# Kernel optimization log

Hardware: AMD Instinct MI355X
Metric: run time of the kernel (lower is better)

Reference implementation:

```python
import jax, jax.numpy as jnp
import numpy as np

B, T, SC, D, N, K, H = 2, 1024, 1024, 2048, 16, 4, 128
SOFTCAP = 50.0
BIG_NEG = -2.3819763e38


def _apply_rope(x, positions, max_wavelength=10_000):
    # x: [B, T, heads, H], positions: [B, T]
    h = x.shape[-1]
    freq_exponents = (2.0 / h) * jnp.arange(h // 2, dtype=jnp.float32)
    timescale = max_wavelength ** freq_exponents
    radians = positions[..., None].astype(jnp.float32) / timescale  # [B,T,H/2]
    radians = radians[..., None, :]  # [B,T,1,H/2]
    sin, cos = jnp.sin(radians), jnp.cos(radians)
    x1, x2 = jnp.split(x, 2, axis=-1)
    out = jnp.concatenate([x1 * cos - x2 * sin, x2 * cos + x1 * sin], axis=-1)
    return out.astype(x.dtype)


def setup_inputs() -> dict:
    key = jax.random.key(0)
    ks = jax.random.split(key, 6)
    x = jax.random.normal(ks[0], (B, T, D), jnp.float32)
    # new-token positions follow the cache: SC .. SC+T-1
    positions = jnp.broadcast_to(SC + jnp.arange(T, dtype=jnp.int32), (B, T))
    # causal mask over concatenated [cache | new] keys
    q_pos = SC + jnp.arange(T)
    k_pos = jnp.arange(SC + T)
    attn_mask = jnp.broadcast_to(
        (k_pos[None, :] <= q_pos[:, None])[None, None], (B, 1, T, SC + T)
    )
    cache_k = jax.random.normal(ks[1], (B, SC, K, H), jnp.float32)
    cache_v = jax.random.normal(ks[2], (B, SC, K, H), jnp.float32)
    wq = jax.random.normal(ks[3], (N, D, H), jnp.float32) * (D ** -0.5)
    wkv = jax.random.normal(ks[4], (2, K, D, H), jnp.float32) * (D ** -0.5)
    wout = jax.random.normal(ks[5], (N, H, D), jnp.float32) * ((N * H) ** -0.5)
    return {"x": x, "positions": positions, "attn_mask": attn_mask,
            "cache_k": cache_k, "cache_v": cache_v,
            "wq": wq, "wkv": wkv, "wout": wout}


def reference(x, positions, attn_mask, cache_k, cache_v, wq, wkv, wout):
    dtype = x.dtype
    h = wq.shape[-1]
    k_heads = wkv.shape[1]
    # projections (GQA path: separate q and fused kv einsums)
    q = jnp.einsum('BTD,NDH->BTNH', x, wq.astype(dtype))
    kv = jnp.einsum('BSD,cKDH->cBSKH', x, wkv.astype(dtype))
    k, v = kv[0], kv[1]
    # RoPE then query pre-attn scaling (rsqrt_head_dim)
    q = _apply_rope(q, positions) * (h ** -0.5)
    k = _apply_rope(k, positions)
    # KV cache concat along sequence axis
    k = jnp.concatenate([cache_k.astype(dtype), k], axis=1)
    v = jnp.concatenate([cache_v.astype(dtype), v], axis=1)
    b, t, n, _ = q.shape
    g = n // k_heads
    q = q.reshape(b, t, k_heads, g, h)  # B T K G H
    logits = jnp.einsum('BTKGH,BSKH->BKGTS', q, k,
                        preferred_element_type=jnp.float32)
    # tanh logits softcap
    logits = jnp.tanh(logits / SOFTCAP) * SOFTCAP
    masked = jnp.where(attn_mask[:, :, None, :, :], logits, BIG_NEG)
    probs = jax.nn.softmax(masked, axis=-1).astype(dtype)
    encoded = jnp.einsum('BKGTS,BSKH->BTKGH', probs, v)
    encoded = encoded.reshape(b, t, n, h)
    out = jnp.einsum('BTNH,NHD->BTD', encoded, wout.astype(dtype))
    return out
```

## Files before the change

### kernel.cpp

```cpp
#include <hip/hip_runtime.h>
#include <stdint.h>
#include <stddef.h>


typedef __bf16 bf16_t;
typedef __bf16 bf16x8 __attribute__((ext_vector_type(8)));
typedef __bf16 bf16x4 __attribute__((ext_vector_type(4)));
typedef float  f32x4  __attribute__((ext_vector_type(4)));

#define GLDS16(gsrc, ldst)                                                      \
  __builtin_amdgcn_global_load_lds(                                             \
      (const __attribute__((address_space(1))) void*)(gsrc),                    \
      (__attribute__((address_space(3))) void*)(ldst), 16, 0, 0)

__global__ __launch_bounds__(256)
void k_prep(const float* __restrict__ x, bf16_t* __restrict__ xb,
            const float* __restrict__ wq, const float* __restrict__ wkv,
            const float* __restrict__ wout,
            bf16_t* __restrict__ w1t, bf16_t* __restrict__ wot) {
  __shared__ bf16_t tile[64][65];
  const int blk = blockIdx.x;
  const int tid = threadIdx.x;
  if (blk < 4096) {
    int i = blk * 256 + tid;
    f32x4 v = *(const f32x4*)(x + (size_t)i * 4);
    bf16x4 o;
    o[0] = (bf16_t)v[0]; o[1] = (bf16_t)v[1]; o[2] = (bf16_t)v[2]; o[3] = (bf16_t)v[3];
    *(bf16x4*)(xb + (size_t)i * 4) = o;
    return;
  }
  const float* s; bf16_t* d; int R, C, bx, by;
  if (blk < 5120) {
    int local = blk - 4096;
    int z = local >> 6, rem = local & 63;
    by = rem >> 1; bx = rem & 1;
    R = 2048; C = 128;
    s = wq + (size_t)z * 2048 * 128;
    d = w1t + (size_t)z * 128 * 2048;
  } else if (blk < 5632) {
    int local = blk - 5120;
    int z = local >> 6, rem = local & 63;
    by = rem >> 1; bx = rem & 1;
    R = 2048; C = 128;
    s = wkv + (size_t)z * 2048 * 128;
    d = w1t + (size_t)2048 * 2048 + (size_t)z * 128 * 2048;
  } else {
    int local = blk - 5632;
    bx = local & 31; by = local >> 5;
    R = 2048; C = 2048;
    s = wout; d = wot;
  }
  const int c0 = bx * 64, r0 = by * 64;
#pragma unroll
  for (int it = 0; it < 16; ++it) {
    int idx = it * 256 + tid;
    int rl = idx >> 6, cl = idx & 63;
    tile[rl][cl] = (bf16_t)s[(size_t)(r0 + rl) * C + (c0 + cl)];
  }
  __syncthreads();
#pragma unroll
  for (int it = 0; it < 16; ++it) {
    int idx = it * 256 + tid;
    int cl = idx >> 6, rl = idx & 63;
    d[(size_t)(c0 + cl) * R + (r0 + rl)] = tile[rl][cl];
  }
}

template <typename CT>
__global__ __launch_bounds__(512)
void k_gemm_bt(const bf16_t* __restrict__ A, const bf16_t* __restrict__ Bt,
               CT* __restrict__ C, int M, int N, int Kd) {
  __shared__ char gsm[65536];
  const int tid = threadIdx.x;
  const int w = tid >> 6, l = tid & 63;
  const int wq = w & 3, wr = wq >> 1, wc = wq & 1, wk = w >> 2;
  const int lr = l & 15, lk = l >> 4;
  const int nwg = gridDim.x * gridDim.y;
  const int bid = blockIdx.y * gridDim.x + blockIdx.x;
  const int cpx = nwg >> 3;
  const int sid = (bid & 7) * cpx + (bid >> 3);
  const int row0 = (sid % gridDim.x) * 128;
  const int col0 = (sid / gridDim.x) * 128;

  auto stage = [&](int buf, int k0) {
#pragma unroll
    for (int inst = 0; inst < 2; ++inst) {
      uint32_t oo = (uint32_t)(inst * 8192 + tid * 16);
      uint32_t r  = oo >> 7;
      uint32_t kb = (oo ^ (((oo >> 7) & 7u) << 4)) & 127u;
      GLDS16((const char*)(A + (size_t)(row0 + r) * Kd + k0) + kb,
             gsm + buf * 16384 + oo);
      GLDS16((const char*)(Bt + (size_t)(col0 + r) * Kd + k0) + kb,
             gsm + 32768 + buf * 16384 + oo);
    }
  };

  f32x4 acc[4][4] = {};
  stage(0, 0);
  asm volatile("s_waitcnt vmcnt(0)" ::: "memory");
  __builtin_amdgcn_s_barrier();
  int cur = 0;
  for (int k0 = 0; k0 < Kd; k0 += 64) {
    if (k0 + 64 < Kd) stage(cur ^ 1, k0 + 64);
    const char* Ab = gsm + cur * 16384;
    const char* Bb = gsm + 32768 + cur * 16384;
    bf16x8 af[4], bfr[4];
#pragma unroll
    for (int m = 0; m < 4; ++m) {
      uint32_t r = (uint32_t)(wr * 64 + m * 16 + lr);
      uint32_t a = (r * 128u + (uint32_t)(wk * 64 + lk * 16)) ^ ((r & 7u) << 4);
      af[m] = *(const bf16x8*)(Ab + a);
    }
#pragma unroll
    for (int n = 0; n < 4; ++n) {
      uint32_t r = (uint32_t)(wc * 64 + n * 16 + lr);
      uint32_t a = (r * 128u + (uint32_t)(wk * 64 + lk * 16)) ^ ((r & 7u) << 4);
      bfr[n] = *(const bf16x8*)(Bb + a);
    }
    __builtin_amdgcn_s_setprio(1);
#pragma unroll
    for (int m = 0; m < 4; ++m)
#pragma unroll
      for (int n = 0; n < 4; ++n)
        acc[m][n] = __builtin_amdgcn_mfma_f32_16x16x32_bf16(af[m], bfr[n], acc[m][n], 0, 0, 0);
    __builtin_amdgcn_s_setprio(0);
    asm volatile("s_waitcnt vmcnt(0)" ::: "memory");
    __builtin_amdgcn_s_barrier();
    __builtin_amdgcn_sched_barrier(0);
    cur ^= 1;
  }
  if (wk == 1) {
#pragma unroll
    for (int m = 0; m < 4; ++m)
#pragma unroll
      for (int n = 0; n < 4; ++n)
        *(f32x4*)(gsm + wq * 16384 + ((m * 4 + n) * 64 + l) * 16) = acc[m][n];
  }
  __syncthreads();
  if (wk == 0) {
#pragma unroll
    for (int m = 0; m < 4; ++m) {
      const int rr = row0 + wr * 64 + m * 16 + lk * 4;
#pragma unroll
      for (int n = 0; n < 4; ++n) {
        f32x4 o = *(const f32x4*)(gsm + wq * 16384 + ((m * 4 + n) * 64 + l) * 16);
        const int cc = col0 + wc * 64 + n * 16 + lr;
        CT* cp = C + (size_t)rr * N + cc;
#pragma unroll
        for (int j = 0; j < 4; ++j) cp[(size_t)j * N] = (CT)(acc[m][n][j] + o[j]);
      }
    }
  }
}

__global__ __launch_bounds__(256)
void k_pre2(const bf16_t* __restrict__ qkv, const int* __restrict__ positions,
            const float* __restrict__ ck, const float* __restrict__ cv,
            bf16_t* __restrict__ Qr, bf16_t* __restrict__ Kf, bf16_t* __restrict__ Vt) {
  __shared__ char shm[16512];
  const int blk = blockIdx.x;
  const int tid = threadIdx.x;
  if (blk < 2048) {
    const int row = blk;
    const int b = row >> 10, t = row & 1023;
    float* cs = (float*)shm;
    float* sn = (float*)shm + 64;
    if (tid < 64) {
      float fe = (float)tid * (2.0f / 128.0f);
      float rad = (float)positions[row] * __builtin_amdgcn_exp2f(-fe * 13.287712379549449f);
      sn[tid] = __sinf(rad);
      cs[tid] = __cosf(rad);
    }
    __syncthreads();
    const bf16_t* rowp = qkv + (size_t)row * 3072;
    const float qs = 0.08838834764831845f;
#pragma unroll
    for (int it = 0; it < 8; ++it) {
      int idx = it * 256 + tid;
      int n = idx >> 7, hh = idx & 127;
      int hp = hh & 63;
      float x1 = (float)rowp[n * 128 + hp];
      float x2 = (float)rowp[n * 128 + 64 + hp];
      float o = (hh < 64) ? (x1 * cs[hp] - x2 * sn[hp]) : (x2 * cs[hp] + x1 * sn[hp]);
      Qr[(((size_t)b * 16 + n) * 1024 + t) * 128 + hh] = (bf16_t)(o * qs);
    }
#pragma unroll
    for (int it = 0; it < 2; ++it) {
      int idx = it * 256 + tid;
      int kh = idx >> 7, hh = idx & 127;
      int hp = hh & 63;
      float x1 = (float)rowp[2048 + kh * 128 + hp];
      float x2 = (float)rowp[2048 + kh * 128 + 64 + hp];
      float o = (hh < 64) ? (x1 * cs[hp] - x2 * sn[hp]) : (x2 * cs[hp] + x1 * sn[hp]);
      Kf[(((size_t)b * 4 + kh) * 2048 + 1024 + t) * 128 + hh] = (bf16_t)o;
    }
    return;
  }
  if (blk < 4096) {
    const int row = blk - 2048;
    const int b = row >> 10, s = row & 1023;
    const float* src = ck + (size_t)row * 512;
#pragma unroll
    for (int it = 0; it < 2; ++it) {
      int idx = it * 256 + tid;
      int kh = idx >> 7, hh = idx & 127;
      Kf[(((size_t)b * 4 + kh) * 2048 + s) * 128 + hh] = (bf16_t)src[idx];
    }
    return;
  }
  {
    const int local = blk - 4096;
    const int s0 = (local & 31) * 64;
    const int bk = local >> 5;
    const int b = bk >> 2, kh = bk & 3;
    bf16_t (*vt)[129] = (bf16_t(*)[129])shm;
#pragma unroll
    for (int it = 0; it < 32; ++it) {
      int idx = it * 256 + tid;
      int sl = idx >> 7, hh = idx & 127;
      int s = s0 + sl;
      vt[sl][hh] = (s < 1024)
        ? (bf16_t)cv[(((size_t)b * 1024 + s) * 4 + kh) * 128 + hh]
        : qkv[((size_t)b * 1024 + (s - 1024)) * 3072 + 2560 + kh * 128 + hh];
    }
    __syncthreads();
#pragma unroll
    for (int it = 0; it < 32; ++it) {
      int idx = it * 256 + tid;
      int hh = idx >> 6, sl = idx & 63;
      Vt[((size_t)bk * 128 + hh) * 2048 + s0 + sl] = vt[sl][hh];
    }
  }
}

__global__ __launch_bounds__(512)
void k_attn(const bf16_t* __restrict__ Qr, const bf16_t* __restrict__ Kf,
            const bf16_t* __restrict__ Vt, bf16_t* __restrict__ enc) {
  __shared__ char smem[74240];
  const int bid = blockIdx.y * gridDim.x + blockIdx.x;
  const int sid = (bid & 7) * 64 + (bid >> 3);
  const int qsel = sid & 15;
  const int bn = sid >> 4;
  const int qblk = ((bn >> 1) & 1) ? (15 - qsel) : qsel;
  const int b = bn >> 4, n = bn & 15;
  const int kh = n >> 2;
  const int tid = threadIdx.x;
  const int w = tid >> 6, l = tid & 63;
  const int qg = w & 1, sw = w >> 1;
  const int window = sw >> 1, hg = sw & 1;
  const int lr = l & 15, lk = l >> 4;
  const bf16_t* Kbase = Kf + ((size_t)b * 4 + kh) * 2048 * 128;
  const bf16_t* Vbase = Vt + ((size_t)b * 4 + kh) * 128 * 2048;
  float* psL = (float*)(smem + 73728);

  bf16x8 aq[2][4];
#pragma unroll
  for (int qf = 0; qf < 2; ++qf) {
    const bf16_t* qp = Qr + ((size_t)bn * 1024 + qblk * 64 + qg * 32 + qf * 16 + lr) * 128;
#pragma unroll
    for (int kk = 0; kk < 4; ++kk) aq[qf][kk] = *(const bf16x8*)(qp + kk * 32 + lk * 8);
  }

  auto stageK = [&](int buf, int s0) {
#pragma unroll
    for (int inst = 0; inst < 2; ++inst) {
      uint32_t oo = (uint32_t)(inst * 8192 + tid * 16);
      uint32_t r  = oo >> 8;
      uint32_t kb = (oo ^ (((oo >> 8) & 7u) << 4)) & 255u;
      GLDS16((const char*)(Kbase + (size_t)(s0 + r) * 128) + kb,
             smem + buf * 16384 + oo);
    }
  };
  auto stageV = [&](int buf, int s0) {
#pragma unroll
    for (int inst = 0; inst < 2; ++inst) {
      uint32_t oo = (uint32_t)(inst * 8192 + tid * 16);
      uint32_t r  = oo >> 7;
      uint32_t sb = (oo ^ (((oo >> 7) & 7u) << 4)) & 127u;
      GLDS16((const char*)(Vbase + (size_t)r * 2048 + s0) + sb,
             smem + 32768 + buf * 16384 + oo);
    }
  };

  char* Pq = smem + 65536 + qg * 4096;
  f32x4 acc[2][4] = {};
  float psum[2] = {0.f, 0.f};
  const int ntiles = 17 + qblk;
  const int qglob0 = 1024 + qblk * 64 + qg * 32 + lr;

  if (tid < 64) psL[tid] = 0.f;
  stageK(0, 0);
  stageV(0, 0);
  asm volatile("s_waitcnt vmcnt(0)" ::: "memory");
  __builtin_amdgcn_s_barrier();
  int cur = 0;

  for (int st = 0; st < ntiles; ++st) {
    const int s0 = st * 64;
    if (st + 1 < ntiles) {
      stageK(cur ^ 1, s0 + 64);
      stageV(cur ^ 1, s0 + 64);
    }
    const char* Kc = smem + cur * 16384;
    const char* Vc = smem + 32768 + cur * 16384;

    f32x4 sacc[2] = {};
    __builtin_amdgcn_s_setprio(1);
#pragma unroll
    for (int kk = 0; kk < 4; ++kk) {
      uint32_t r = (uint32_t)(sw * 16 + lr);
      uint32_t a = (r * 256u + (uint32_t)(kk * 64 + lk * 16)) ^ ((r & 7u) << 4);
      bf16x8 ak = *(const bf16x8*)(Kc + a);
      sacc[0] = __builtin_amdgcn_mfma_f32_16x16x32_bf16(ak, aq[0][kk], sacc[0], 0, 0, 0);
      sacc[1] = __builtin_amdgcn_mfma_f32_16x16x32_bf16(ak, aq[1][kk], sacc[1], 0, 0, 0);
    }
    __builtin_amdgcn_s_setprio(0);

    const bool last = (st == ntiles - 1);
#pragma unroll
    for (int qf = 0; qf < 2; ++qf) {
      const int q = qf * 16 + lr;
      bf16x4 pq;
#pragma unroll
      for (int j = 0; j < 4; ++j) {
        float lg = sacc[qf][j];
        float t  = lg * 1.4426950408889634f;
        float u  = 1.0f - (lg * lg) * (1.0f / 7500.0f);
        float p  = __builtin_amdgcn_exp2f(t * u);
        if (last) {
          int sg = s0 + sw * 16 + lk * 4 + j;
          if (sg > qglob0 + qf * 16) p = 0.0f;
        }
        psum[qf] += p;
        pq[j] = (bf16_t)p;
      }
      uint32_t a = ((uint32_t)(q * 128) + (uint32_t)(sw * 32 + lk * 8)) ^ (((uint32_t)lr & 7u) << 4);
      *(bf16x4*)(Pq + a) = pq;
    }
    asm volatile("s_waitcnt lgkmcnt(0)" ::: "memory");
    __builtin_amdgcn_s_barrier();
    __builtin_amdgcn_sched_barrier(0);

    {
      bf16x8 pa[2];
#pragma unroll
      for (int qf = 0; qf < 2; ++qf) {
        uint32_t a = ((uint32_t)((qf * 16 + lr) * 128) + (uint32_t)(window * 64 + lk * 16)) ^ (((uint32_t)lr & 7u) << 4);
        pa[qf] = *(const bf16x8*)(Pq + a);
      }
      __builtin_amdgcn_s_setprio(1);
#pragma unroll
      for (int i = 0; i < 4; ++i) {
        uint32_t h = (uint32_t)((hg * 4 + i) * 16 + lr);
        uint32_t va = (h * 128u + (uint32_t)(window * 64 + lk * 16)) ^ ((h & 7u) << 4);
        bf16x8 bv = *(const bf16x8*)(Vc + va);
        acc[0][i] = __builtin_amdgcn_mfma_f32_16x16x32_bf16(pa[0], bv, acc[0][i], 0, 0, 0);
        acc[1][i] = __builtin_amdgcn_mfma_f32_16x16x32_bf16(pa[1], bv, acc[1][i], 0, 0, 0);
      }
      __builtin_amdgcn_s_setprio(0);
    }
    asm volatile("s_waitcnt vmcnt(0)" ::: "memory");
    __builtin_amdgcn_s_barrier();
    __builtin_amdgcn_sched_barrier(0);
    cur ^= 1;
  }

  float ps0 = psum[0];
  ps0 += __shfl_xor(ps0, 16); ps0 += __shfl_xor(ps0, 32);
  float ps1 = psum[1];
  ps1 += __shfl_xor(ps1, 16); ps1 += __shfl_xor(ps1, 32);
  if (l < 16) {
    atomicAdd(&psL[qg * 32 + lr], ps0);
    atomicAdd(&psL[qg * 32 + 16 + lr], ps1);
  }
  float* accL = (float*)smem;
  if (window == 1) {
    char* sb = (char*)(accL) + (qg * 2 + hg) * 8192;
#pragma unroll
    for (int qf = 0; qf < 2; ++qf)
#pragma unroll
      for (int i = 0; i < 4; ++i) {
        uint32_t a = (uint32_t)(l * 128) + ((uint32_t)((qf * 4 + i) * 16) ^ (((uint32_t)l & 7u) << 4));
        *(f32x4*)(sb + a) = acc[qf][i];
      }
  }
  __syncthreads();
  if (window == 0) {
    char* sb = (char*)(accL) + (qg * 2 + hg) * 8192;
    float inv[2][4];
#pragma unroll
    for (int qf = 0; qf < 2; ++qf)
#pragma unroll
      for (int j = 0; j < 4; ++j)
        inv[qf][j] = 1.0f / (psL[qg * 32 + qf * 16 + lk * 4 + j] + 1e-30f);
#pragma unroll
    for (int qf = 0; qf < 2; ++qf) {
#pragma unroll
      for (int i = 0; i < 4; ++i) {
        uint32_t a = (uint32_t)(l * 128) + ((uint32_t)((qf * 4 + i) * 16) ^ (((uint32_t)l & 7u) << 4));
        f32x4 o2 = *(const f32x4*)(sb + a);
        const int col = n * 128 + (hg * 4 + i) * 16 + lr;
#pragma unroll
        for (int j = 0; j < 4; ++j) {
          int trow = qblk * 64 + qg * 32 + qf * 16 + lk * 4 + j;
          enc[((size_t)b * 1024 + trow) * 2048 + col] =
              (bf16_t)((acc[qf][i][j] + o2[j]) * inv[qf][j]);
        }
      }
    }
  }
}

extern "C" void kernel_launch(void* const* d_in, const int* in_sizes, int n_in,
                              void* d_out, int out_size, void* d_ws, size_t ws_size,
                              hipStream_t stream) {
  (void)in_sizes; (void)n_in; (void)out_size; (void)ws_size;
  const float* x    = (const float*)d_in[0];
  const int*   pos  = (const int*)d_in[1];
  const float* ck   = (const float*)d_in[3];
  const float* cv   = (const float*)d_in[4];
  const float* wq   = (const float*)d_in[5];
  const float* wkv  = (const float*)d_in[6];
  const float* wout = (const float*)d_in[7];
  float* out = (float*)d_out;

  char* p = (char*)d_ws;
  bf16_t* xb  = (bf16_t*)p; p += (size_t)2048 * 2048 * 2;
  bf16_t* w1t = (bf16_t*)p; p += (size_t)3072 * 2048 * 2;
  bf16_t* qkv = (bf16_t*)p; p += (size_t)2048 * 3072 * 2;
  bf16_t* Qr  = (bf16_t*)p; p += (size_t)32 * 1024 * 128 * 2;
  bf16_t* Kf  = (bf16_t*)p; p += (size_t)8 * 2048 * 128 * 2;
  bf16_t* Vt  = (bf16_t*)p; p += (size_t)8 * 128 * 2048 * 2;
  bf16_t* enc = (bf16_t*)p; p += (size_t)2048 * 2048 * 2;
  bf16_t* wot = (bf16_t*)p; p += (size_t)2048 * 2048 * 2;

  k_prep<<<6656, 256, 0, stream>>>(x, xb, wq, wkv, wout, w1t, wot);
  k_gemm_bt<bf16_t><<<dim3(16, 24), 512, 0, stream>>>(xb, w1t, qkv, 2048, 3072, 2048);
  k_pre2<<<4352, 256, 0, stream>>>(qkv, pos, ck, cv, Qr, Kf, Vt);
  k_attn<<<dim3(16, 32), 512, 0, stream>>>(Qr, Kf, Vt, enc);
  k_gemm_bt<float><<<dim3(16, 16), 512, 0, stream>>>(enc, wot, out, 2048, 2048, 2048);
}
```

Before: 130.9 us.

## Feed softmax probabilities directly from registers into PV MFMA, dropping LDS round-trip

The probabilities computed from the QK^T accumulator are reused in registers as the A operand of 16x16x16 bf16 MFMAs against V. This removes the LDS write/read of P and one barrier per KV tile. Each wave now keeps the full head dimension (8 accumulator tiles instead of 4), doubling accumulator registers. A two-stage LDS reduction across the four S-split waves replaces the previous single-stage combine. The kernel uses half-width MFMAs, adds a launch-bounds occupancy hint and shrinks shared memory, at the cost of higher register pressure and a longer epilogue.

```diff
diff --git a/kernel.cpp b/kernel.cpp
--- a/kernel.cpp
+++ b/kernel.cpp
@@ -7,11 +7,24 @@
 typedef __bf16 bf16x8 __attribute__((ext_vector_type(8)));
 typedef __bf16 bf16x4 __attribute__((ext_vector_type(4)));
 typedef float  f32x4  __attribute__((ext_vector_type(4)));
+typedef short  short4_t __attribute__((ext_vector_type(4)));
 
 #define GLDS16(gsrc, ldst)                                                      \
   __builtin_amdgcn_global_load_lds(                                             \
       (const __attribute__((address_space(1))) void*)(gsrc),                    \
       (__attribute__((address_space(3))) void*)(ldst), 16, 0, 0)
+
+static __device__ __forceinline__ f32x4 mfma_pv16(bf16x4 a, bf16x4 b, f32x4 c) {
+#if __has_builtin(__builtin_amdgcn_mfma_f32_16x16x16_bf16)
+  return __builtin_amdgcn_mfma_f32_16x16x16_bf16(a, b, c, 0, 0, 0);
+#elif __has_builtin(__builtin_amdgcn_mfma_f32_16x16x16bf16_1k)
+  return __builtin_amdgcn_mfma_f32_16x16x16bf16_1k(
+      __builtin_bit_cast(short4_t, a), __builtin_bit_cast(short4_t, b), c, 0, 0, 0);
+#else
+  asm("v_mfma_f32_16x16x16_bf16 %0, %1, %2, %0" : "+v"(c) : "v"(a), "v"(b));
+  return c;
+#endif
+}
 
 __global__ __launch_bounds__(256)
 void k_prep(const float* __restrict__ x, bf16_t* __restrict__ xb,
@@ -233,10 +246,10 @@
   }
 }
 
-__global__ __launch_bounds__(512)
+__global__ __launch_bounds__(512, 4)
 void k_attn(const bf16_t* __restrict__ Qr, const bf16_t* __restrict__ Kf,
             const bf16_t* __restrict__ Vt, bf16_t* __restrict__ enc) {
-  __shared__ char smem[74240];
+  __shared__ char smem[65792];
   const int bid = blockIdx.y * gridDim.x + blockIdx.x;
   const int sid = (bid & 7) * 64 + (bid >> 3);
   const int qsel = sid & 15;
@@ -247,11 +260,10 @@
   const int tid = threadIdx.x;
   const int w = tid >> 6, l = tid & 63;
   const int qg = w & 1, sw = w >> 1;
-  const int window = sw >> 1, hg = sw & 1;
   const int lr = l & 15, lk = l >> 4;
   const bf16_t* Kbase = Kf + ((size_t)b * 4 + kh) * 2048 * 128;
   const bf16_t* Vbase = Vt + ((size_t)b * 4 + kh) * 128 * 2048;
-  float* psL = (float*)(smem + 73728);
+  float* psL = (float*)(smem + 65536);
 
   bf16x8 aq[2][4];
 #pragma unroll
@@ -282,8 +294,7 @@
     }
   };
 
-  char* Pq = smem + 65536 + qg * 4096;
-  f32x4 acc[2][4] = {};
+  f32x4 acc[2][8] = {};
   float psum[2] = {0.f, 0.f};
   const int ntiles = 17 + qblk;
   const int qglob0 = 1024 + qblk * 64 + qg * 32 + lr;
@@ -317,10 +328,9 @@
     __builtin_amdgcn_s_setprio(0);
 
     const bool last = (st == ntiles - 1);
+    bf16x4 pa[2];
 #pragma unroll
     for (int qf = 0; qf < 2; ++qf) {
-      const int q = qf * 16 + lr;
-      bf16x4 pq;
 #pragma unroll
       for (int j = 0; j < 4; ++j) {
         float lg = sacc[qf][j];
@@ -332,33 +342,21 @@
           if (sg > qglob0 + qf * 16) p = 0.0f;
         }
         psum[qf] += p;
-        pq[j] = (bf16_t)p;
+        pa[qf][j] = (bf16_t)p;
       }
-      uint32_t a = ((uint32_t)(q * 128) + (uint32_t)(sw * 32 + lk * 8)) ^ (((uint32_t)lr & 7u) << 4);
-      *(bf16x4*)(Pq + a) = pq;
-    }
-    asm volatile("s_waitcnt lgkmcnt(0)" ::: "memory");
-    __builtin_amdgcn_s_barrier();
-    __builtin_amdgcn_sched_barrier(0);
-
-    {
-      bf16x8 pa[2];
-#pragma unroll
-      for (int qf = 0; qf < 2; ++qf) {
-        uint32_t a = ((uint32_t)((qf * 16 + lr) * 128) + (uint32_t)(window * 64 + lk * 16)) ^ (((uint32_t)lr & 7u) << 4);
-        pa[qf] = *(const bf16x8*)(Pq + a);
-      }
-      __builtin_amdgcn_s_setprio(1);
-#pragma unroll
-      for (int i = 0; i < 4; ++i) {
-        uint32_t h = (uint32_t)((hg * 4 + i) * 16 + lr);
-        uint32_t va = (h * 128u + (uint32_t)(window * 64 + lk * 16)) ^ ((h & 7u) << 4);
-        bf16x8 bv = *(const bf16x8*)(Vc + va);
-        acc[0][i] = __builtin_amdgcn_mfma_f32_16x16x32_bf16(pa[0], bv, acc[0][i], 0, 0, 0);
-        acc[1][i] = __builtin_amdgcn_mfma_f32_16x16x32_bf16(pa[1], bv, acc[1][i], 0, 0, 0);
-      }
-      __builtin_amdgcn_s_setprio(0);
-    }
+    }
+
+    __builtin_amdgcn_s_setprio(1);
+#pragma unroll
+    for (int hf = 0; hf < 8; ++hf) {
+      uint32_t h = (uint32_t)(hf * 16 + lr);
+      uint32_t va = h * 128u + (((uint32_t)(sw * 32 + lk * 8)) ^ ((h & 7u) << 4));
+      bf16x4 bv = *(const bf16x4*)(Vc + va);
+      acc[0][hf] = mfma_pv16(pa[0], bv, acc[0][hf]);
+      acc[1][hf] = mfma_pv16(pa[1], bv, acc[1][hf]);
+    }
+    __builtin_amdgcn_s_setprio(0);
+
     asm volatile("s_waitcnt vmcnt(0)" ::: "memory");
     __builtin_amdgcn_s_barrier();
     __builtin_amdgcn_sched_barrier(0);
@@ -374,19 +372,38 @@
     atomicAdd(&psL[qg * 32 + 16 + lr], ps1);
   }
   float* accL = (float*)smem;
-  if (window == 1) {
-    char* sb = (char*)(accL) + (qg * 2 + hg) * 8192;
+  if (sw >= 2) {
+    char* sb = (char*)accL + (qg * 2 + (sw - 2)) * 16384;
 #pragma unroll
     for (int qf = 0; qf < 2; ++qf)
 #pragma unroll
-      for (int i = 0; i < 4; ++i) {
-        uint32_t a = (uint32_t)(l * 128) + ((uint32_t)((qf * 4 + i) * 16) ^ (((uint32_t)l & 7u) << 4));
-        *(f32x4*)(sb + a) = acc[qf][i];
+      for (int hf = 0; hf < 8; ++hf)
+        *(f32x4*)(sb + ((qf * 8 + hf) * 64 + l) * 16) = acc[qf][hf];
+  }
+  __syncthreads();
+  if (sw < 2) {
+    const char* sb = (const char*)accL + (qg * 2 + sw) * 16384;
+#pragma unroll
+    for (int qf = 0; qf < 2; ++qf)
+#pragma unroll
+      for (int hf = 0; hf < 8; ++hf) {
+        f32x4 v = *(const f32x4*)(sb + ((qf * 8 + hf) * 64 + l) * 16);
+        acc[qf][hf][0] += v[0]; acc[qf][hf][1] += v[1];
+        acc[qf][hf][2] += v[2]; acc[qf][hf][3] += v[3];
       }
   }
   __syncthreads();
-  if (window == 0) {
-    char* sb = (char*)(accL) + (qg * 2 + hg) * 8192;
+  if (sw == 1) {
+    char* sb = (char*)accL + (qg * 2) * 16384;
+#pragma unroll
+    for (int qf = 0; qf < 2; ++qf)
+#pragma unroll
+      for (int hf = 0; hf < 8; ++hf)
+        *(f32x4*)(sb + ((qf * 8 + hf) * 64 + l) * 16) = acc[qf][hf];
+  }
+  __syncthreads();
+  if (sw == 0) {
+    const char* sb = (const char*)accL + (qg * 2) * 16384;
     float inv[2][4];
 #pragma unroll
     for (int qf = 0; qf < 2; ++qf)
@@ -396,15 +413,14 @@
 #pragma unroll
     for (int qf = 0; qf < 2; ++qf) {
 #pragma unroll
-      for (int i = 0; i < 4; ++i) {
-        uint32_t a = (uint32_t)(l * 128) + ((uint32_t)((qf * 4 + i) * 16) ^ (((uint32_t)l & 7u) << 4));
-        f32x4 o2 = *(const f32x4*)(sb + a);
-        const int col = n * 128 + (hg * 4 + i) * 16 + lr;
+      for (int hf = 0; hf < 8; ++hf) {
+        f32x4 v = *(const f32x4*)(sb + ((qf * 8 + hf) * 64 + l) * 16);
+        const int col = n * 128 + hf * 16 + lr;
 #pragma unroll
         for (int j = 0; j < 4; ++j) {
           int trow = qblk * 64 + qg * 32 + qf * 16 + lk * 4 + j;
           enc[((size_t)b * 1024 + trow) * 2048 + col] =
-              (bf16_t)((acc[qf][i][j] + o2[j]) * inv[qf][j]);
+              (bf16_t)((acc[qf][hf][j] + v[j]) * inv[qf][j]);
         }
       }
     }
```

After: 154.6 us. 18.1% more time.
